# Kernel tuning notes

Measured on AMD Instinct MI355X. Metric: run time of the kernel, lower is better.

## Reference

```python
import jax, jax.numpy as jnp
import numpy as np

B, N, D_IN, D_OUT, R = 8, 2048, 256, 256, 4


def setup_inputs() -> dict:
    key = jax.random.key(0)
    k1, k2, k3, k4 = jax.random.split(key, 4)
    x = jax.random.normal(k1, (B, N, D_IN), dtype=jnp.float32)
    adj = jnp.zeros((1,), dtype=jnp.float32)  # unused by the module
    # relation-type matrix: 0 = no edge, 1..R = relation id
    relation = jax.random.randint(k2, (B, N, N), 0, R + 1, dtype=jnp.int32)
    weight = jax.random.normal(k3, (R, D_IN, D_OUT), dtype=jnp.float32) * 0.05
    bias = jax.random.normal(k4, (D_OUT,), dtype=jnp.float32) * 0.05
    return {"x": x, "adj": adj, "relation": relation, "weight": weight, "bias": bias}


def reference(x, adj, relation, weight, bias):
    # Binary per-relation adjacency masks: [R, B, N, N]
    rel_ids = jnp.arange(1, weight.shape[0] + 1, dtype=relation.dtype)
    masks = (relation[None] == rel_ids[:, None, None, None]).astype(x.dtype)
    # Aggregate neighbors per relation: h[r] = A_r @ x  -> [R, B, N, D_in]
    h = jnp.einsum('rbnm,bmd->rbnd', masks, x)
    # Per-relation output transform, summed over relations: [B, N, D_out]
    y = jnp.einsum('rbnd,rdo->bno', h, weight)
    return y + bias
```

## Files before the change

kernel.cpp:

```cpp
#include <hip/hip_runtime.h>
#include <hip/hip_bf16.h>
#include <stdint.h>

typedef uint32_t u32;
typedef uint64_t u64;
typedef __bf16 bf16x8 __attribute__((ext_vector_type(8)));
typedef float f32x4 __attribute__((ext_vector_type(4)));
typedef u32 u32x4 __attribute__((ext_vector_type(4)));

#define NB 8
#define NN 2048
#define DIN 256
#define DOUT 256
#define NR 4
#define KTOT (NN * NR)

#define XW_BYTES   (NB * DOUT * KTOT * 2)
#define PART_BYTES (NB * NN * DOUT * 4)
#define WT_BYTES   (NR * DIN * DOUT * 2)
#define PART_ELEMS (NB * NN * DOUT)

__device__ __forceinline__ ushort f2bf(float f) {
  union { float f; u32 u; } c; c.f = f;
  return (ushort)((c.u + 0x7FFFu + ((c.u >> 16) & 1u)) >> 16);
}

__device__ __forceinline__ float bf2f(ushort u) {
  union { u32 i; float f; } c; c.i = ((u32)u) << 16; return c.f;
}

__device__ __forceinline__ void gload_lds16(const void* g, void* l) {
  __builtin_amdgcn_global_load_lds(
      (const __attribute__((address_space(1))) u32*)g,
      (__attribute__((address_space(3))) u32*)l, 16, 0, 0);
}

__device__ __forceinline__ u32 relmask(int v) {
  return v ? (0xFFu << (((u32)(v - 1) & 3u) * 8u)) : 0u;
}

__global__ void k0_wT(const float* __restrict__ w, ushort* __restrict__ wT) {
  int i = blockIdx.x * 256 + threadIdx.x;
  int o = i & 255, d = (i >> 8) & 255, r = i >> 16;
  wT[(r * DOUT + o) * DIN + d] = f2bf(w[i]);
}

__global__ __launch_bounds__(512) void k1_xw(const float* __restrict__ x,
                                             const ushort* __restrict__ wT,
                                             ushort* __restrict__ xwT) {
  __shared__ char smem[65536];
  ushort* As = (ushort*)smem;
  ushort* Bs = (ushort*)(smem + 4096);
  const int t = threadIdx.x, l = t & 63, w = t >> 6;
  const int r = w >> 1, oh = w & 1;
  const int blk = blockIdx.x;
  const int b = blk >> 6, rest = blk & 63, mc = rest >> 1, ot = rest & 1;

  f32x4 acc[4][4] = {};
  const int arow = t >> 3, adc = (t & 7) << 2;
  const float* xg = x + ((size_t)(b * NN + mc * 64 + arow) * DIN + adc);

  for (int s = 0; s < 8; ++s) {
    const int d0 = s * 32;
    float4 xv = *(const float4*)(xg + d0);
    ushort4 a4;
    a4.x = f2bf(xv.x); a4.y = f2bf(xv.y); a4.z = f2bf(xv.z); a4.w = f2bf(xv.w);
    *(ushort4*)(As + arow * 32 + adc) = a4;
#pragma unroll
    for (int i = 0; i < 4; ++i) {
      int off = i * 4096 + t * 8;
      int rr = off >> 12, rem = off & 4095, o = rem >> 5, dd = rem & 31;
      const ushort* src = wT + ((size_t)(rr * DOUT + ot * 128 + o) * DIN + d0 + dd);
      gload_lds16(src, Bs + off);
    }
    __syncthreads();
    bf16x8 af[4];
#pragma unroll
    for (int fm = 0; fm < 4; ++fm)
      af[fm] = *(const bf16x8*)(As + (fm * 16 + (l & 15)) * 32 + (l >> 4) * 8);
#pragma unroll
    for (int fo = 0; fo < 4; ++fo) {
      bf16x8 bf = *(const bf16x8*)(Bs + (size_t)(r * 128 + oh * 64 + fo * 16 + (l & 15)) * 32 + (l >> 4) * 8);
#pragma unroll
      for (int fm = 0; fm < 4; ++fm)
        acc[fm][fo] = __builtin_amdgcn_mfma_f32_16x16x32_bf16(af[fm], bf, acc[fm][fo], 0, 0, 0);
    }
    __syncthreads();
  }
  ushort* Cs = (ushort*)smem;
#pragma unroll
  for (int fm = 0; fm < 4; ++fm)
#pragma unroll
    for (int fo = 0; fo < 4; ++fo)
#pragma unroll
      for (int j = 0; j < 4; ++j) {
        int o_loc = oh * 64 + fo * 16 + (l & 15);
        int ml = fm * 16 + (l >> 4) * 4 + j;
        Cs[o_loc * 256 + ml * 4 + r] = f2bf(acc[fm][fo][j]);
      }
  __syncthreads();
#pragma unroll
  for (int i = 0; i < 8; ++i) {
    int el = (i * 512 + t) * 8;
    int o_loc = el >> 8, kp = el & 255;
    *(uint4*)(xwT + (size_t)(b * DOUT + ot * 128 + o_loc) * KTOT + mc * 256 + kp) =
        *(const uint4*)(Cs + el);
  }
}

__global__ __launch_bounds__(512, 2) void k2_v5(const int* __restrict__ rel,
                                                const ushort* __restrict__ xwT,
                                                ushort* __restrict__ partb) {
  __shared__ char smem[98304];
  const int t = threadIdx.x, l = t & 63, w = t >> 6;
  const int wm = w >> 2, wn = w & 3;
  const int logical = (blockIdx.x & 7) * 32 + (blockIdx.x >> 3);
  const int b = logical >> 5;
  const int nt = (logical >> 2) & 7;
  const int ks = logical & 3;

  f32x4 acc[8][4] = {};
  const int fr = l & 15, fq = l >> 4;
  const int rswz = (fr & 7) << 4;

  char* const Ab0 = smem;
  char* const Ab1 = smem + 16384;
  char* const Bb0 = smem + 32768;
  char* const Bb1 = smem + 65536;

  const int arow = t >> 1, half = t & 1;
  const int* relg = rel + ((size_t)(b * NN + nt * 256 + arow)) * NN + ks * 512 + half * 8;
  char* const rowA0 = Ab0 + arow * 64;
  char* const rowA1 = Ab1 + arow * 64;

  const int brow = t >> 3;
  const int kd = (((t & 7) ^ ((t >> 3) & 7)) << 3);
  const ushort* xwb = xwT + (size_t)b * DOUT * KTOT + ks * 2048;

  int4 rs0a, rs0b, rs1a, rs1b;

#define GLD_ALL(S, BB)                                                         \
  {                                                                            \
    _Pragma("unroll") for (int i = 0; i < 4; ++i)                              \
      gload_lds16(xwb + (size_t)(brow + 64 * i) * KTOT + (S) * 64 + kd,        \
                  (BB) + i * 8192 + t * 16);                                   \
  }

#define RELLOAD(S, RA, RB)                                                     \
  RA = *(const int4*)(relg + (S) * 16);                                        \
  RB = *(const int4*)(relg + (S) * 16 + 4);

#define EXPAND_M(ROWP, V0, V1)                                                 \
  {                                                                            \
    int vv[8] = {V0.x, V0.y, V0.z, V0.w, V1.x, V1.y, V1.z, V1.w};              \
    _Pragma("unroll") for (int jj = 0; jj < 4; ++jj) {                         \
      u64 mw = (u64)relmask(vv[2 * jj]) | ((u64)relmask(vv[2 * jj + 1]) << 32);\
      *(u64*)((ROWP) + (((half * 4 + jj) ^ (arow & 7)) * 8)) = mw;             \
    }                                                                          \
  }

#define RDB(BV, BB, KK)                                                        \
  _Pragma("unroll") for (int fo = 0; fo < 4; ++fo)                             \
    BV[fo] = *(const bf16x8*)((BB) + (wn * 64 + fo * 16 + fr) * 128 +          \
                              (((KK) * 64 + fq * 16) ^ rswz));

#define RDA_K(AR, AB, KK)                                                      \
  _Pragma("unroll") for (int f = 0; f < 8; ++f)                                \
    AR[f] = *(const int2*)((AB) + (wm * 128 + f * 16 + fr) * 64 +              \
                           ((((KK) * 4 + fq) ^ (fr & 7)) * 8));

#define MFMA1(FM, Q, BV)                                                       \
  {                                                                            \
    u32x4 uu;                                                                  \
    uu.x = __builtin_amdgcn_perm((u32)(Q).x, (u32)(Q).x, 0x01010000u) & 0x3F803F80u; \
    uu.y = __builtin_amdgcn_perm((u32)(Q).x, (u32)(Q).x, 0x03030202u) & 0x3F803F80u; \
    uu.z = __builtin_amdgcn_perm((u32)(Q).y, (u32)(Q).y, 0x01010000u) & 0x3F803F80u; \
    uu.w = __builtin_amdgcn_perm((u32)(Q).y, (u32)(Q).y, 0x03030202u) & 0x3F803F80u; \
    union { u32x4 u; bf16x8 b; } cv; cv.u = uu;                                \
    _Pragma("unroll") for (int fo = 0; fo < 4; ++fo)                           \
      acc[FM][fo] = __builtin_amdgcn_mfma_f32_16x16x32_bf16(                   \
          cv.b, BV[fo], acc[FM][fo], 0, 0, 0);                                 \
  }

#define MFMAH(AR, BV)                                                          \
  __builtin_amdgcn_s_setprio(1);                                               \
  _Pragma("unroll") for (int f = 0; f < 8; ++f) MFMA1(f, AR[f], BV);           \
  __builtin_amdgcn_s_setprio(0);

#define ENDF(VMS)                                                              \
  asm volatile("s_waitcnt vmcnt(" VMS ") lgkmcnt(0)" ::: "memory");            \
  __builtin_amdgcn_s_barrier();                                                \
  __builtin_amdgcn_sched_barrier(0);

#define STEP(S, P, Q, STG, REL, EXP, VMS)                                      \
  {                                                                            \
    bf16x8 bv0[4], bv1[4];                                                     \
    int2 a0[8], a1[8];                                                         \
    RDB(bv0, Bb##P, 0);                                                        \
    RDA_K(a0, Ab##P, 0);                                                       \
    if (STG) { GLD_ALL((S) + 1, Bb##Q); }                                      \
    __builtin_amdgcn_sched_barrier(0);                                         \
    if (REL) { RELLOAD((S) + 2, rs##P##a, rs##P##b); }                         \
    __builtin_amdgcn_sched_barrier(0);                                         \
    MFMAH(a0, bv0);                                                            \
    RDB(bv1, Bb##P, 1);                                                        \
    RDA_K(a1, Ab##P, 1);                                                       \
    if (EXP) { EXPAND_M(rowA##Q, rs##Q##a, rs##Q##b); }                        \
    MFMAH(a1, bv1);                                                            \
    ENDF(VMS);                                                                 \
  }

  GLD_ALL(0, Bb0);
  __builtin_amdgcn_sched_barrier(0);
  RELLOAD(0, rs0a, rs0b);
  RELLOAD(1, rs1a, rs1b);
  EXPAND_M(rowA0, rs0a, rs0b);
  ENDF("4");

  for (int s = 0; s < 30; s += 2) {
    STEP(s, 0, 1, 1, 1, 1, "2");
    STEP(s + 1, 1, 0, 1, 1, 1, "2");
  }
  STEP(30, 0, 1, 1, 0, 1, "0");
  {
    bf16x8 bv0[4], bv1[4];
    int2 a0[8], a1[8];
    RDB(bv0, Bb1, 0);
    RDA_K(a0, Ab1, 0);
    MFMAH(a0, bv0);
    RDB(bv1, Bb1, 1);
    RDA_K(a1, Ab1, 1);
    MFMAH(a1, bv1);
  }

  ushort* dst = partb + (size_t)ks * PART_ELEMS;
#pragma unroll
  for (int fm = 0; fm < 8; ++fm)
#pragma unroll
    for (int fo = 0; fo < 4; ++fo) {
      int n = nt * 256 + wm * 128 + fm * 16 + fq * 4;
      int o = wn * 64 + fo * 16 + fr;
#pragma unroll
      for (int j = 0; j < 4; ++j)
        dst[(size_t)(b * NN + n + j) * DOUT + o] = f2bf(acc[fm][fo][j]);
    }
#undef STEP
#undef ENDF
#undef MFMAH
#undef MFMA1
#undef RDA_K
#undef RDB
#undef EXPAND_M
#undef RELLOAD
#undef GLD_ALL
}

__global__ void k3_sum(float* __restrict__ out, const ushort* __restrict__ partb,
                       const float* __restrict__ bias) {
  int i = blockIdx.x * 256 + threadIdx.x;
  float4 s = ((const float4*)bias)[i & 63];
#pragma unroll
  for (int p = 0; p < 4; ++p) {
    ushort4 v = ((const ushort4*)(partb + (size_t)p * PART_ELEMS))[i];
    s.x += bf2f(v.x); s.y += bf2f(v.y); s.z += bf2f(v.z); s.w += bf2f(v.w);
  }
  ((float4*)out)[i] = s;
}

__global__ __launch_bounds__(256, 2) void k2_r4(const int* __restrict__ rel,
                                                const ushort* __restrict__ xwT,
                                                float* __restrict__ out,
                                                float* __restrict__ part) {
  __shared__ char smem[81920];
  const int t = threadIdx.x, l = t & 63, w = t >> 6;
  const int wr = w >> 1, wc = w & 1;
  const int logical = (blockIdx.x & 7) * 64 + (blockIdx.x >> 3);
  const int b = logical >> 6;
  const int nt = (logical >> 2) & 15;
  const int ks = (logical >> 1) & 1;
  const int ot = logical & 1;

  f32x4 acc[4][4] = {};
  const int arow = t >> 1, half = t & 1;
  const int* relg = rel + ((size_t)(b * NN + nt * 128 + arow) * NN + ks * 1024 + half * 8);
  const ushort* xwb = xwT + (size_t)(b * DOUT + ot * 128) * KTOT + ks * 4096;

  char* const Ab0 = smem;
  char* const Ab1 = smem + 16384;
  char* const Bb0 = smem + 32768;
  char* const Bb1 = smem + 49152;
  char* const Bb2 = smem + 65536;

  const int brow = t >> 3;
  const int kd = (((t & 7) ^ ((t >> 3) & 7)) << 3);
  const int aswz = (arow & 7) << 4;
  const int fr = l & 15, fq = l >> 4;
  const int rswz = (fr & 7) << 4;

  int4 rsA0, rsB0, rsA1, rsB1;

#define STAGE_B(S, BBASE)                                                      \
  {                                                                            \
    _Pragma("unroll") for (int i = 0; i < 4; ++i)                              \
      gload_lds16(xwb + (size_t)(brow + 32 * i) * KTOT + (S) * 64 + kd,        \
                  (BBASE) + i * 4096 + t * 16);                                \
  }
#define RELLOAD(S, RA, RB)                                                     \
  RA = *(const int4*)(relg + (S) * 16);                                        \
  RB = *(const int4*)(relg + (S) * 16 + 4);
#define EXPAND_A(ABASE, V0, V1)                                                \
  {                                                                            \
    char* rowp = (ABASE) + arow * 128;                                         \
    int vv[8] = {V0.x, V0.y, V0.z, V0.w, V1.x, V1.y, V1.z, V1.w};              \
    _Pragma("unroll") for (int p = 0; p < 4; ++p) {                            \
      int va = vv[2 * p], vb = vv[2 * p + 1];                                  \
      u32 sa = ((u32)(va - 1) & 3u) * 16u;                                     \
      u32 sb = ((u32)(vb - 1) & 3u) * 16u;                                     \
      u64 ha = va ? (0x3F80ull << sa) : 0ull;                                  \
      u64 hb = vb ? (0x3F80ull << sb) : 0ull;                                  \
      u32x4 e = {(u32)ha, (u32)(ha >> 32), (u32)hb, (u32)(hb >> 32)};          \
      *(u32x4*)(rowp + ((half * 64 + p * 16) ^ aswz)) = e;                     \
    }                                                                          \
  }
#define BARV6()                                                                \
  asm volatile("s_waitcnt vmcnt(6) lgkmcnt(0)" ::: "memory");                  \
  __builtin_amdgcn_s_barrier();                                                \
  __builtin_amdgcn_sched_barrier(0);
#define BARV0()                                                                \
  asm volatile("s_waitcnt vmcnt(0) lgkmcnt(0)" ::: "memory");                  \
  __builtin_amdgcn_s_barrier();                                                \
  __builtin_amdgcn_sched_barrier(0);
#define MFMA_STEP(AC, BC)                                                      \
  __builtin_amdgcn_s_setprio(1);                                               \
  _Pragma("unroll") for (int kk = 0; kk < 2; ++kk) {                           \
    bf16x8 af[4], bfv[4];                                                      \
    const int colb = (kk * 64 + fq * 16) ^ rswz;                               \
    _Pragma("unroll") for (int fm = 0; fm < 4; ++fm)                           \
      af[fm] = *(const bf16x8*)((AC) + (wr * 64 + fm * 16 + fr) * 128 + colb); \
    _Pragma("unroll") for (int fo = 0; fo < 4; ++fo)                           \
      bfv[fo] = *(const bf16x8*)((BC) + (wc * 64 + fo * 16 + fr) * 128 + colb);\
    _Pragma("unroll") for (int fm = 0; fm < 4; ++fm)                           \
      _Pragma("unroll") for (int fo = 0; fo < 4; ++fo)                         \
        acc[fm][fo] = __builtin_amdgcn_mfma_f32_16x16x32_bf16(                 \
            af[fm], bfv[fo], acc[fm][fo], 0, 0, 0);                            \
  }                                                                            \
  __builtin_amdgcn_s_setprio(0);
#define BODY(S, ACUR, BCUR, ANXT, RLA, RLB, RCA, RCB, BSTG)                    \
  {                                                                            \
    STAGE_B((S) + 2, BSTG);                                                    \
    RELLOAD((S) + 2, RLA, RLB);                                                \
    MFMA_STEP(ACUR, BCUR);                                                     \
    EXPAND_A(ANXT, RCA, RCB);                                                  \
    BARV6();                                                                   \
  }

  STAGE_B(0, Bb0);
  RELLOAD(0, rsA0, rsB0);
  STAGE_B(1, Bb1);
  RELLOAD(1, rsA1, rsB1);
  EXPAND_A(Ab0, rsA0, rsB0);
  BARV6();

  for (int s = 0; s < 60; s += 6) {
    BODY(s + 0, Ab0, Bb0, Ab1, rsA0, rsB0, rsA1, rsB1, Bb2);
    BODY(s + 1, Ab1, Bb1, Ab0, rsA1, rsB1, rsA0, rsB0, Bb0);
    BODY(s + 2, Ab0, Bb2, Ab1, rsA0, rsB0, rsA1, rsB1, Bb1);
    BODY(s + 3, Ab1, Bb0, Ab0, rsA1, rsB1, rsA0, rsB0, Bb2);
    BODY(s + 4, Ab0, Bb1, Ab1, rsA0, rsB0, rsA1, rsB1, Bb0);
    BODY(s + 5, Ab1, Bb2, Ab0, rsA1, rsB1, rsA0, rsB0, Bb1);
  }
  BODY(60, Ab0, Bb0, Ab1, rsA0, rsB0, rsA1, rsB1, Bb2);
  BODY(61, Ab1, Bb1, Ab0, rsA1, rsB1, rsA0, rsB0, Bb0);
  {
    MFMA_STEP(Ab0, Bb2);
    EXPAND_A(Ab1, rsA1, rsB1);
    BARV0();
  }
  {
    MFMA_STEP(Ab1, Bb0);
  }

  float* dst = ks ? part : out;
#pragma unroll
  for (int fm = 0; fm < 4; ++fm)
#pragma unroll
    for (int fo = 0; fo < 4; ++fo) {
      int n = nt * 128 + wr * 64 + fm * 16 + fq * 4;
      int o = ot * 128 + wc * 64 + fo * 16 + fr;
#pragma unroll
      for (int j = 0; j < 4; ++j)
        dst[(size_t)(b * NN + n + j) * DOUT + o] = acc[fm][fo][j];
    }
#undef BODY
#undef MFMA_STEP
#undef BARV6
#undef BARV0
#undef EXPAND_A
#undef RELLOAD
#undef STAGE_B
}

__global__ void k3_r4(float* __restrict__ out, const float* __restrict__ part,
                      const float* __restrict__ bias) {
  int i = blockIdx.x * 256 + threadIdx.x;
  float4 o = ((const float4*)out)[i];
  float4 p = ((const float4*)part)[i];
  float4 bv = ((const float4*)bias)[i & 63];
  float4 rr;
  rr.x = o.x + p.x + bv.x;
  rr.y = o.y + p.y + bv.y;
  rr.z = o.z + p.z + bv.z;
  rr.w = o.w + p.w + bv.w;
  ((float4*)out)[i] = rr;
}

extern "C" void kernel_launch(void* const* d_in, const int* in_sizes, int n_in,
                              void* d_out, int out_size, void* d_ws, size_t ws_size,
                              hipStream_t stream) {
  const float* x = (const float*)d_in[0];
  const int* rel = (const int*)d_in[2];
  const float* wgt = (const float*)d_in[3];
  const float* bias = (const float*)d_in[4];
  float* out = (float*)d_out;
  char* ws = (char*)d_ws;

  const size_t partb_bytes = (size_t)PART_ELEMS * 2 * 4;
  const size_t need_big = (size_t)XW_BYTES + partb_bytes + WT_BYTES;
  if (ws_size >= need_big) {
    ushort* xwT = (ushort*)ws;
    ushort* partb = (ushort*)(ws + XW_BYTES);
    ushort* wT = (ushort*)(ws + XW_BYTES + partb_bytes);
    k0_wT<<<1024, 256, 0, stream>>>(wgt, wT);
    k1_xw<<<512, 512, 0, stream>>>(x, wT, xwT);
    k2_v5<<<256, 512, 0, stream>>>(rel, xwT, partb);
    k3_sum<<<4096, 256, 0, stream>>>(out, partb, bias);
  } else {
    ushort* xwT = (ushort*)ws;
    float* part = (float*)(ws + XW_BYTES);
    ushort* wT = (ushort*)(ws + XW_BYTES + PART_BYTES);
    k0_wT<<<1024, 256, 0, stream>>>(wgt, wT);
    k1_xw<<<512, 512, 0, stream>>>(x, wT, xwT);
    k2_r4<<<512, 256, 0, stream>>>(rel, xwT, out, part);
    k3_r4<<<4096, 256, 0, stream>>>(out, part, bias);
  }
}
```

Before: 115.1 us.

## Split k2 output tile across two blocks of 256 threads with smaller LDS

```diff
diff --git a/kernel.cpp b/kernel.cpp
--- a/kernel.cpp
+++ b/kernel.cpp
@@ -108,15 +108,16 @@
   }
 }
 
-__global__ __launch_bounds__(512, 2) void k2_v5(const int* __restrict__ rel,
+__global__ __launch_bounds__(256, 2) void k2_v6(const int* __restrict__ rel,
                                                 const ushort* __restrict__ xwT,
                                                 ushort* __restrict__ partb) {
-  __shared__ char smem[98304];
+  __shared__ char smem[65536];
   const int t = threadIdx.x, l = t & 63, w = t >> 6;
-  const int wm = w >> 2, wn = w & 3;
-  const int logical = (blockIdx.x & 7) * 32 + (blockIdx.x >> 3);
-  const int b = logical >> 5;
-  const int nt = (logical >> 2) & 7;
+  const int wm = w >> 1, wn = w & 1;
+  const int logical = (blockIdx.x & 7) * 64 + (blockIdx.x >> 3);
+  const int b = logical >> 6;
+  const int nt = (logical >> 3) & 7;
+  const int ot = (logical >> 2) & 1;
   const int ks = logical & 3;
 
   f32x4 acc[8][4] = {};
@@ -126,36 +127,41 @@
   char* const Ab0 = smem;
   char* const Ab1 = smem + 16384;
   char* const Bb0 = smem + 32768;
-  char* const Bb1 = smem + 65536;
+  char* const Bb1 = smem + 49152;
 
   const int arow = t >> 1, half = t & 1;
   const int* relg = rel + ((size_t)(b * NN + nt * 256 + arow)) * NN + ks * 512 + half * 8;
-  char* const rowA0 = Ab0 + arow * 64;
-  char* const rowA1 = Ab1 + arow * 64;
+  const u32 awx = ((u32)arow & 7u) ^ (((u32)arow >> 3) & 3u);
+  char* const rowA0a = Ab0 + arow * 64;
+  char* const rowA0b = Ab0 + (arow + 128) * 64;
+  char* const rowA1a = Ab1 + arow * 64;
+  char* const rowA1b = Ab1 + (arow + 128) * 64;
 
   const int brow = t >> 3;
   const int kd = (((t & 7) ^ ((t >> 3) & 7)) << 3);
-  const ushort* xwb = xwT + (size_t)b * DOUT * KTOT + ks * 2048;
-
-  int4 rs0a, rs0b, rs1a, rs1b;
-
-#define GLD_ALL(S, BB)                                                         \
+  const ushort* xwb = xwT + (size_t)(b * DOUT + ot * 128) * KTOT + ks * 2048;
+
+  int4 rs0a, rs0b, rs0c, rs0d, rs1a, rs1b, rs1c, rs1d;
+
+#define GLD_B(S, BB)                                                           \
   {                                                                            \
     _Pragma("unroll") for (int i = 0; i < 4; ++i)                              \
-      gload_lds16(xwb + (size_t)(brow + 64 * i) * KTOT + (S) * 64 + kd,        \
-                  (BB) + i * 8192 + t * 16);                                   \
-  }
-
-#define RELLOAD(S, RA, RB)                                                     \
+      gload_lds16(xwb + (size_t)(brow + 32 * i) * KTOT + (S) * 64 + kd,        \
+                  (BB) + i * 4096 + t * 16);                                   \
+  }
+
+#define RELLOAD(S, RA, RB, RC, RD)                                             \
   RA = *(const int4*)(relg + (S) * 16);                                        \
-  RB = *(const int4*)(relg + (S) * 16 + 4);
-
-#define EXPAND_M(ROWP, V0, V1)                                                 \
+  RB = *(const int4*)(relg + (S) * 16 + 4);                                    \
+  RC = *(const int4*)(relg + (size_t)128 * NN + (S) * 16);                     \
+  RD = *(const int4*)(relg + (size_t)128 * NN + (S) * 16 + 4);
+
+#define EXPROW(ROWP, V0, V1)                                                   \
   {                                                                            \
     int vv[8] = {V0.x, V0.y, V0.z, V0.w, V1.x, V1.y, V1.z, V1.w};              \
     _Pragma("unroll") for (int jj = 0; jj < 4; ++jj) {                         \
       u64 mw = (u64)relmask(vv[2 * jj]) | ((u64)relmask(vv[2 * jj + 1]) << 32);\
-      *(u64*)((ROWP) + (((half * 4 + jj) ^ (arow & 7)) * 8)) = mw;             \
+      *(u64*)((ROWP) + ((((u32)(half * 4 + jj)) ^ awx) * 8)) = mw;             \
     }                                                                          \
   }
 
@@ -167,7 +173,7 @@
 #define RDA_K(AR, AB, KK)                                                      \
   _Pragma("unroll") for (int f = 0; f < 8; ++f)                                \
     AR[f] = *(const int2*)((AB) + (wm * 128 + f * 16 + fr) * 64 +              \
-                           ((((KK) * 4 + fq) ^ (fr & 7)) * 8));
+        (((((KK) * 4 + fq)) ^ (fr & 7) ^ ((f * 2 + (fr >> 3)) & 3)) * 8));
 
 #define MFMA1(FM, Q, BV)                                                       \
   {                                                                            \
@@ -198,28 +204,30 @@
     int2 a0[8], a1[8];                                                         \
     RDB(bv0, Bb##P, 0);                                                        \
     RDA_K(a0, Ab##P, 0);                                                       \
-    if (STG) { GLD_ALL((S) + 1, Bb##Q); }                                      \
+    if (STG) { GLD_B((S) + 1, Bb##Q); }                                        \
     __builtin_amdgcn_sched_barrier(0);                                         \
-    if (REL) { RELLOAD((S) + 2, rs##P##a, rs##P##b); }                         \
+    if (REL) { RELLOAD((S) + 2, rs##P##a, rs##P##b, rs##P##c, rs##P##d); }     \
     __builtin_amdgcn_sched_barrier(0);                                         \
     MFMAH(a0, bv0);                                                            \
     RDB(bv1, Bb##P, 1);                                                        \
     RDA_K(a1, Ab##P, 1);                                                       \
-    if (EXP) { EXPAND_M(rowA##Q, rs##Q##a, rs##Q##b); }                        \
+    if (EXP) { EXPROW(rowA##Q##a, rs##Q##a, rs##Q##b);                         \
+               EXPROW(rowA##Q##b, rs##Q##c, rs##Q##d); }                       \
     MFMAH(a1, bv1);                                                            \
     ENDF(VMS);                                                                 \
   }
 
-  GLD_ALL(0, Bb0);
+  GLD_B(0, Bb0);
   __builtin_amdgcn_sched_barrier(0);
-  RELLOAD(0, rs0a, rs0b);
-  RELLOAD(1, rs1a, rs1b);
-  EXPAND_M(rowA0, rs0a, rs0b);
+  RELLOAD(0, rs0a, rs0b, rs0c, rs0d);
+  RELLOAD(1, rs1a, rs1b, rs1c, rs1d);
+  EXPROW(rowA0a, rs0a, rs0b);
+  EXPROW(rowA0b, rs0c, rs0d);
   ENDF("4");
 
   for (int s = 0; s < 30; s += 2) {
-    STEP(s, 0, 1, 1, 1, 1, "2");
-    STEP(s + 1, 1, 0, 1, 1, 1, "2");
+    STEP(s, 0, 1, 1, 1, 1, "4");
+    STEP(s + 1, 1, 0, 1, 1, 1, "4");
   }
   STEP(30, 0, 1, 1, 0, 1, "0");
   {
@@ -239,7 +247,7 @@
 #pragma unroll
     for (int fo = 0; fo < 4; ++fo) {
       int n = nt * 256 + wm * 128 + fm * 16 + fq * 4;
-      int o = wn * 64 + fo * 16 + fr;
+      int o = ot * 128 + wn * 64 + fo * 16 + fr;
 #pragma unroll
       for (int j = 0; j < 4; ++j)
         dst[(size_t)(b * NN + n + j) * DOUT + o] = f2bf(acc[fm][fo][j]);
@@ -250,9 +258,9 @@
 #undef MFMA1
 #undef RDA_K
 #undef RDB
-#undef EXPAND_M
+#undef EXPROW
 #undef RELLOAD
-#undef GLD_ALL
+#undef GLD_B
 }
 
 __global__ void k3_sum(float* __restrict__ out, const ushort* __restrict__ partb,
@@ -432,7 +440,7 @@
     ushort* wT = (ushort*)(ws + XW_BYTES + partb_bytes);
     k0_wT<<<1024, 256, 0, stream>>>(wgt, wT);
     k1_xw<<<512, 512, 0, stream>>>(x, wT, xwT);
-    k2_v5<<<256, 512, 0, stream>>>(rel, xwT, partb);
+    k2_v6<<<512, 256, 0, stream>>>(rel, xwT, partb);
     k3_sum<<<4096, 256, 0, stream>>>(out, partb, bias);
   } else {
     ushort* xwT = (ushort*)ws;
```

After: 116.6 us. Within noise of the previous version (+1.3%).
